# Kernel tuning notes

Hardware: AMD Instinct MI355X
Metric: run time of the kernel (lower is better)

Reference implementation:

```python
import jax, jax.numpy as jnp
import numpy as np

DIM = 768
NUM_HEADS = 12
HEAD_DIM = DIM // NUM_HEADS
H, W = 16, 64
HK, WK = 7, 11
N = H * W
B = 8
SCALE = HEAD_DIM ** -0.5


def build_local_mask():
    # Vectorized version of the original nested loop: for each token (h,w),
    # positions inside the hk x wk window are visible (0), others -inf.
    h_idx = np.repeat(np.arange(H), W)  # [N]
    w_idx = np.tile(np.arange(W), H)    # [N]
    hh = np.arange(H + HK - 1)
    ww = np.arange(W + WK - 1)
    in_h = (hh[None, :] >= h_idx[:, None]) & (hh[None, :] < h_idx[:, None] + HK)  # [N, H+hk-1]
    in_w = (ww[None, :] >= w_idx[:, None]) & (ww[None, :] < w_idx[:, None] + WK)  # [N, W+wk-1]
    visible = in_h[:, :, None] & in_w[:, None, :]  # [N, H+hk-1, W+wk-1]
    mask_big = np.where(visible, 0.0, 1.0).astype(np.float32)
    mask_crop = mask_big[:, HK // 2:H + HK // 2, WK // 2:W + WK // 2].reshape(N, N)
    mask = np.where(mask_crop < 1.0, mask_crop, np.float32(-np.inf))  # [N, N]
    return jnp.asarray(mask)[None, None]  # [1, 1, N, N]


def setup_inputs() -> dict:
    key = jax.random.key(0)
    k1, k2, k3 = jax.random.split(key, 3)
    x = jax.random.normal(k1, (B, N, DIM), dtype=jnp.float32)
    w_qkv = jax.random.normal(k2, (3 * DIM, DIM), dtype=jnp.float32) * 0.02  # torch Linear weight [out,in]
    w_proj = jax.random.normal(k3, (DIM, DIM), dtype=jnp.float32) * 0.02
    b_proj = jnp.zeros((DIM,), dtype=jnp.float32)
    mask = build_local_mask()
    return {"x": x, "w_qkv": w_qkv, "w_proj": w_proj, "b_proj": b_proj, "mask": mask}


def reference(x, w_qkv, w_proj, b_proj, mask):
    Bx, Nx, C = x.shape
    qkv = jnp.einsum('bnc,oc->bno', x, w_qkv)  # [B, N, 3*dim]
    qkv = qkv.reshape(Bx, Nx, 3, NUM_HEADS, HEAD_DIM).transpose(2, 0, 3, 1, 4)  # [3,B,h,N,d]
    q, k, v = qkv[0] * SCALE, qkv[1], qkv[2]
    attn = jnp.einsum('bhnd,bhmd->bhnm', q, k) + mask  # [B,h,N,N] with local -inf mask
    attn = jax.nn.softmax(attn, axis=-1)
    out = jnp.einsum('bhnm,bhmd->bhnd', attn, v)  # [B,h,N,d]
    out = out.transpose(0, 2, 1, 3).reshape(Bx, Nx, C)
    out = jnp.einsum('bnc,oc->bno', out, w_proj) + b_proj
    return out
```

## Files before the change

kernel.cpp:

```cpp
#include <hip/hip_runtime.h>
#include <hip/hip_bf16.h>
#include <stdint.h>

typedef __bf16 bf16;
typedef __bf16 bf16x8 __attribute__((ext_vector_type(8)));
typedef __bf16 bf16x4 __attribute__((ext_vector_type(4)));
typedef float f32x4 __attribute__((ext_vector_type(4)));

#define KDIM 768
#define NHEAD 12
#define HDIM 64
#define NTOK 1024
#define BATCH 8

#define SWZ(row, b) ((b) ^ (((row) & 7) << 4))

__device__ __forceinline__ void gl_lds16(const bf16* g, bf16* l) {
    __builtin_amdgcn_global_load_lds((const __attribute__((address_space(1))) void*)g,
                                     (__attribute__((address_space(3))) void*)l, 16, 0, 0);
}

#define G_MFMA(a, b, c) __builtin_amdgcn_mfma_f32_16x16x32_bf16(a, b, c, 0, 0, 0)
#define VMW(N) asm volatile("s_waitcnt vmcnt(" #N ")" ::: "memory")

__global__ void k_cvt_all(const float* __restrict__ x, const float* __restrict__ wq,
                          const float* __restrict__ wp, bf16* __restrict__ xb,
                          bf16* __restrict__ wqb, bf16* __restrict__ wpb) {
    int b = blockIdx.x;
    const float* src;
    bf16* dst;
    int base;
    if (b < 6144)       { src = x;  dst = xb;  base = b; }
    else if (b < 7872)  { src = wq; dst = wqb; base = b - 6144; }
    else                { src = wp; dst = wpb; base = b - 7872; }
    int i = (base * 256 + threadIdx.x) * 4;
    float4 v = *(const float4*)(src + i);
    bf16x4 o;
    o[0] = (bf16)v.x; o[1] = (bf16)v.y; o[2] = (bf16)v.z; o[3] = (bf16)v.w;
    *(bf16x4*)(dst + i) = o;
}


#define TILE64(S, kt) do {                                                      \
    const char* A8 = (const char*)sA[S];                                        \
    const char* B8 = (const char*)sB[S];                                        \
    bf16x8 af[4], bfr[6];                                                       \
    _Pragma("unroll")                                                           \
    for (int m = 0; m < 4; ++m)                                                 \
        af[m] = *(const bf16x8*)(A8 + (wr * 64 + m * 16 + lr) * 128 + k0off);   \
    _Pragma("unroll")                                                           \
    for (int n = 0; n < 6; ++n)                                                 \
        bfr[n] = *(const bf16x8*)(B8 + (wc * 96 + n * 16 + lr) * 128 + k0off);  \
    if ((kt) < 11) {                                                            \
        const bf16* p_ = Ast + (size_t)((kt) + 1) * 64;                         \
        gl_lds16(p_,                      &sA[(S) ^ 1][t * 8]);                 \
        gl_lds16(p_ + (size_t)32 * KDIM,  &sA[(S) ^ 1][t * 8 + 2048]);          \
        gl_lds16(p_ + (size_t)64 * KDIM,  &sA[(S) ^ 1][t * 8 + 4096]);          \
        gl_lds16(p_ + (size_t)96 * KDIM,  &sA[(S) ^ 1][t * 8 + 6144]);          \
    }                                                                           \
    __builtin_amdgcn_s_setprio(1);                                              \
    _Pragma("unroll")                                                           \
    for (int m = 0; m < 4; ++m)                                                 \
        _Pragma("unroll")                                                       \
        for (int n = 0; n < 6; ++n)                                             \
            acc[m][n] = G_MFMA(af[m], bfr[n], acc[m][n]);                       \
    __builtin_amdgcn_s_setprio(0);                                              \
    _Pragma("unroll")                                                           \
    for (int m = 0; m < 4; ++m)                                                 \
        af[m] = *(const bf16x8*)(A8 + (wr * 64 + m * 16 + lr) * 128 + k1off);   \
    _Pragma("unroll")                                                           \
    for (int n = 0; n < 6; ++n)                                                 \
        bfr[n] = *(const bf16x8*)(B8 + (wc * 96 + n * 16 + lr) * 128 + k1off);  \
    if ((kt) < 11) {                                                            \
        const bf16* p_ = Wst + (size_t)((kt) + 1) * 64;                         \
        gl_lds16(p_,                       &sB[(S) ^ 1][t * 8]);                \
        gl_lds16(p_ + (size_t)32 * KDIM,   &sB[(S) ^ 1][t * 8 + 2048]);         \
        gl_lds16(p_ + (size_t)64 * KDIM,   &sB[(S) ^ 1][t * 8 + 4096]);         \
        gl_lds16(p_ + (size_t)96 * KDIM,   &sB[(S) ^ 1][t * 8 + 6144]);         \
        gl_lds16(p_ + (size_t)128 * KDIM,  &sB[(S) ^ 1][t * 8 + 8192]);         \
        gl_lds16(p_ + (size_t)160 * KDIM,  &sB[(S) ^ 1][t * 8 + 10240]);        \
    }                                                                           \
    __builtin_amdgcn_s_setprio(1);                                              \
    _Pragma("unroll")                                                           \
    for (int m = 0; m < 4; ++m)                                                 \
        _Pragma("unroll")                                                       \
        for (int n = 0; n < 6; ++n)                                             \
            acc[m][n] = G_MFMA(af[m], bfr[n], acc[m][n]);                       \
    __builtin_amdgcn_s_setprio(0);                                              \
    VMW(0);                                                                     \
    __builtin_amdgcn_s_barrier();                                               \
} while (0)

#define GEMM64_PRE(A_PTR, W_PTR)                                                \
    const int t = threadIdx.x;                                                  \
    const int lane = t & 63;                                                    \
    const int wv = t >> 6;                                                      \
    const int wr = wv >> 1, wc = wv & 1;                                        \
    const int lr = lane & 15, lg = lane >> 4;                                   \
    const int xorb = (lr & 7) << 4;                                             \
    const int k0off = (lg << 4) ^ xorb;                                         \
    const int k1off = (64 + (lg << 4)) ^ xorb;                                  \
    const int spos = ((t & 7) ^ ((t >> 3) & 7)) * 8;                            \
    const int bm = blockIdx.x, bn = blockIdx.y;                                 \
    const bf16* Ast = (A_PTR) + (size_t)(bm * 128 + (t >> 3)) * KDIM + spos;    \
    const bf16* Wst = (W_PTR) + (size_t)(bn * 192 + (t >> 3)) * KDIM + spos;    \
    f32x4 acc[4][6] = {};                                                       \
    gl_lds16(Ast,                      &sA[0][t * 8]);                          \
    gl_lds16(Ast + (size_t)32 * KDIM,  &sA[0][t * 8 + 2048]);                   \
    gl_lds16(Ast + (size_t)64 * KDIM,  &sA[0][t * 8 + 4096]);                   \
    gl_lds16(Ast + (size_t)96 * KDIM,  &sA[0][t * 8 + 6144]);                   \
    gl_lds16(Wst,                       &sB[0][t * 8]);                         \
    gl_lds16(Wst + (size_t)32 * KDIM,   &sB[0][t * 8 + 2048]);                  \
    gl_lds16(Wst + (size_t)64 * KDIM,   &sB[0][t * 8 + 4096]);                  \
    gl_lds16(Wst + (size_t)96 * KDIM,   &sB[0][t * 8 + 6144]);                  \
    gl_lds16(Wst + (size_t)128 * KDIM,  &sB[0][t * 8 + 8192]);                  \
    gl_lds16(Wst + (size_t)160 * KDIM,  &sB[0][t * 8 + 10240]);                 \
    VMW(0);                                                                     \
    __builtin_amdgcn_s_barrier();                                               \
    _Pragma("unroll 1")                                                         \
    for (int g = 0; g < 6; ++g) {                                               \
        TILE64(0, g * 2);                                                       \
        TILE64(1, g * 2 + 1);                                                   \
    }

__global__ __launch_bounds__(256, 2) void k_gemm_qkv(
    const bf16* __restrict__ A, const bf16* __restrict__ W,
    bf16* __restrict__ qb, bf16* __restrict__ kb, bf16* __restrict__ vb)
{
    __shared__ __attribute__((aligned(16))) bf16 sA[2][8192];
    __shared__ __attribute__((aligned(16))) bf16 sB[2][12288];
    GEMM64_PRE(A, W);

    const float QSC = 0.18033688011112042f;
#pragma unroll
    for (int n = 0; n < 6; ++n) {
        int o = bn * 192 + wc * 96 + n * 16 + lr;
        int s = o / 768;
        int rem = o - s * 768;
        int head = rem >> 6;
        int d = o & 63;
        bf16* dst = (s == 0) ? qb : ((s == 1) ? kb : vb);
        float sc = (s == 0) ? QSC : 1.0f;
#pragma unroll
        for (int m = 0; m < 4; ++m) {
            int grow = bm * 128 + wr * 64 + m * 16 + lg * 4;
            int bidx = grow >> 10;
            int tok = grow & 1023;
            size_t base = (((size_t)bidx * NHEAD + head) * NTOK + tok) * HDIM + d;
#pragma unroll
            for (int r = 0; r < 4; ++r)
                dst[base + (size_t)r * HDIM] = (bf16)(acc[m][n][r] * sc);
        }
    }
}

__global__ __launch_bounds__(256, 2) void k_gemm_proj(
    const bf16* __restrict__ A, const bf16* __restrict__ W,
    const float* __restrict__ bias, float* __restrict__ out)
{
    __shared__ __attribute__((aligned(16))) bf16 sA[2][8192];
    __shared__ __attribute__((aligned(16))) bf16 sB[2][12288];
    GEMM64_PRE(A, W);

#pragma unroll
    for (int n = 0; n < 6; ++n) {
        int col = bn * 192 + wc * 96 + n * 16 + lr;
        float bv = bias[col];
#pragma unroll
        for (int m = 0; m < 4; ++m) {
            int grow = bm * 128 + wr * 64 + m * 16 + lg * 4;
#pragma unroll
            for (int r = 0; r < 4; ++r)
                out[(size_t)(grow + r) * KDIM + col] = acc[m][n][r] + bv;
        }
    }
}

__global__ __launch_bounds__(256) void k_attn(
    const bf16* __restrict__ qbuf, const bf16* __restrict__ kbuf,
    const bf16* __restrict__ vbuf, bf16* __restrict__ ob)
{
    const int x = blockIdx.x;
    const int sub = x >> 3;
    const int bh = (x & 7) * 12 + (sub >> 4);
    const int qblk = sub & 15;
    const int head = bh % NHEAD, bidx = bh / NHEAD;
    const bf16* Q  = qbuf + (size_t)bh * NTOK * HDIM;
    const bf16* Kp = kbuf + (size_t)bh * NTOK * HDIM;
    const bf16* Vp = vbuf + (size_t)bh * NTOK * HDIM;

    const int t = threadIdx.x, lane = t & 63, wv = t >> 6;
    const int lr = lane & 15, lg = lane >> 4, lkb = lg * 8;

    __shared__ bf16 Ks[2][64 * 64];
    __shared__ bf16 vT[2][64 * 64];
    __shared__ bf16 pls[4][16 * 64];

    {
        bf16x8 z = {};
        *(bf16x8*)&pls[wv][lane * 16] = z;
        *(bf16x8*)&pls[wv][lane * 16 + 8] = z;
    }

    bf16x8 qf[2];
#pragma unroll
    for (int ks = 0; ks < 2; ++ks)
        qf[ks] = *(const bf16x8*)(Q + (size_t)(qblk * 64 + wv * 16 + lr) * HDIM + ks * 32 + lkb);

    f32x4 acc[4] = {};
    float lrow[4] = {0.f, 0.f, 0.f, 0.f};

    const int kh0 = (qblk - 3 < 0) ? 0 : qblk - 3;
    const int kh1 = (qblk + 3 > 15) ? 15 : qblk + 3;

    const int sj = t >> 2;
    const int sd = (t & 3) * 16;

    const bf16* ks0 = Kp + (size_t)(kh0 * 64 + sj) * HDIM + sd;
    const bf16* vs0 = Vp + (size_t)(kh0 * 64 + sj) * HDIM + sd;
    bf16x8 gk0 = *(const bf16x8*)ks0, gk1 = *(const bf16x8*)(ks0 + 8);
    bf16x8 gv0 = *(const bf16x8*)vs0, gv1 = *(const bf16x8*)(vs0 + 8);

    char* pb8 = (char*)pls[wv];
    const int wq0 = wv * 16 + lg * 4;
    int cur = 0;

    for (int kh = kh0; kh <= kh1; ++kh) {
        char* kb8 = (char*)Ks[cur];
        char* vb8 = (char*)vT[cur];
        {
            int kbo = sj * 128 + sd * 2;
            *(bf16x8*)(kb8 + SWZ(sj, kbo)) = gk0;
            *(bf16x8*)(kb8 + SWZ(sj, kbo + 16)) = gk1;
        }
#pragma unroll
        for (int ii = 0; ii < 8; ++ii) {
            int d = sd + ii;
            *(bf16*)(vb8 + SWZ(d, (d << 7) + (sj << 1))) = gv0[ii];
        }
#pragma unroll
        for (int ii = 0; ii < 8; ++ii) {
            int d = sd + 8 + ii;
            *(bf16*)(vb8 + SWZ(d, (d << 7) + (sj << 1))) = gv1[ii];
        }
        if (kh < kh1) {
            const bf16* kn = Kp + (size_t)((kh + 1) * 64 + sj) * HDIM + sd;
            const bf16* vn = Vp + (size_t)((kh + 1) * 64 + sj) * HDIM + sd;
            gk0 = *(const bf16x8*)kn; gk1 = *(const bf16x8*)(kn + 8);
            gv0 = *(const bf16x8*)vn; gv1 = *(const bf16x8*)(vn + 8);
        }
        asm volatile("s_waitcnt lgkmcnt(0)" ::: "memory");
        __builtin_amdgcn_s_barrier();

        float psum[4] = {0.f, 0.f, 0.f, 0.f};
#pragma unroll
        for (int jj = 0; jj < 3; ++jj) {
            int j = wv - 1 + jj;
            if (j >= 0 && j <= 3) {
                int key = j * 16 + lr;
                int kbase = key * 128;
                bf16x8 kf0 = *(const bf16x8*)(kb8 + SWZ(key, kbase + lg * 16));
                bf16x8 kf1 = *(const bf16x8*)(kb8 + SWZ(key, kbase + 64 + lg * 16));
                f32x4 sv = {};
                sv = G_MFMA(qf[0], kf0, sv);
                sv = G_MFMA(qf[1], kf1, sv);
#pragma unroll
                for (int r = 0; r < 4; ++r) {
                    int dw = wq0 + r - key;
                    float p = (dw >= -5 && dw <= 5) ? exp2f(sv[r]) : 0.0f;
                    psum[r] += p;
                    int row = lg * 4 + r;
                    *(bf16*)(pb8 + SWZ(row, row * 128 + key * 2)) = (bf16)p;
                }
            }
        }
#pragma unroll
        for (int r = 0; r < 4; ++r) lrow[r] += psum[r];

        bf16x8 pf0 = *(const bf16x8*)(pb8 + SWZ(lr, lr * 128 + lg * 16));
        bf16x8 pf1 = *(const bf16x8*)(pb8 + SWZ(lr, lr * 128 + 64 + lg * 16));
#pragma unroll
        for (int dt = 0; dt < 4; ++dt) {
            int vrow = dt * 16 + lr;
            bf16x8 vf0 = *(const bf16x8*)(vb8 + SWZ(vrow, vrow * 128 + lg * 16));
            bf16x8 vf1 = *(const bf16x8*)(vb8 + SWZ(vrow, vrow * 128 + 64 + lg * 16));
            acc[dt] = G_MFMA(pf0, vf0, acc[dt]);
            acc[dt] = G_MFMA(pf1, vf1, acc[dt]);
        }
        cur ^= 1;
    }

#pragma unroll
    for (int off = 1; off < 16; off <<= 1)
#pragma unroll
        for (int r = 0; r < 4; ++r) lrow[r] += __shfl_xor(lrow[r], off);

#pragma unroll
    for (int r = 0; r < 4; ++r) {
        float inv = 1.0f / lrow[r];
        int tok = qblk * 64 + wv * 16 + lg * 4 + r;
        size_t rowbase = ((size_t)bidx * NTOK + tok) * KDIM + head * HDIM;
#pragma unroll
        for (int dt = 0; dt < 4; ++dt)
            ob[rowbase + dt * 16 + lr] = (bf16)(acc[dt][r] * inv);
    }
}

extern "C" void kernel_launch(void* const* d_in, const int* in_sizes, int n_in,
                              void* d_out, int out_size, void* d_ws, size_t ws_size,
                              hipStream_t stream) {
    const float* x      = (const float*)d_in[0];
    const float* w_qkv  = (const float*)d_in[1];
    const float* w_proj = (const float*)d_in[2];
    const float* b_proj = (const float*)d_in[3];
    float* out = (float*)d_out;

    char* ws = (char*)d_ws;
    bf16* xb  = (bf16*)(ws);
    bf16* wqb = (bf16*)(ws + 12582912);
    bf16* wpb = (bf16*)(ws + 16121856);
    bf16* qb  = (bf16*)(ws + 17301504);
    bf16* kb  = (bf16*)(ws + 29884416);
    bf16* vb  = (bf16*)(ws + 42467328);
    bf16* aob = (bf16*)(ws + 55050240);

    hipLaunchKernelGGL(k_cvt_all, dim3(8448), dim3(256), 0, stream, x, w_qkv, w_proj, xb, wqb, wpb);
    hipLaunchKernelGGL(k_gemm_qkv, dim3(64, 12), dim3(256), 0, stream, xb, wqb, qb, kb, vb);
    hipLaunchKernelGGL(k_attn,     dim3(1536), dim3(256), 0, stream, qb, kb, vb, aob);
    hipLaunchKernelGGL(k_gemm_proj, dim3(64, 4), dim3(256), 0, stream, aob, wpb, b_proj, out);
}
```

Before: 91.20 us.

## Process two query blocks per attention workgroup to share K/V tile loads

The attention kernel now uses 512-thread workgroups covering two adjacent 64-row query blocks, with eight waves split into two groups of four. Each K/V key block is loaded and transposed into LDS once and consumed by both query groups. This halves the grid and cuts redundant global K/V loads and LDS staging per query block. In exchange, the loop spans one extra key block, during which half the waves sit idle at the barrier. Occupancy may also change with the larger workgroup and LDS footprint.

```diff
diff --git a/kernel.cpp b/kernel.cpp
--- a/kernel.cpp
+++ b/kernel.cpp
@@ -176,25 +176,27 @@
     }
 }
 
-__global__ __launch_bounds__(256) void k_attn(
+__global__ __launch_bounds__(512) void k_attn(
     const bf16* __restrict__ qbuf, const bf16* __restrict__ kbuf,
     const bf16* __restrict__ vbuf, bf16* __restrict__ ob)
 {
     const int x = blockIdx.x;
     const int sub = x >> 3;
-    const int bh = (x & 7) * 12 + (sub >> 4);
-    const int qblk = sub & 15;
+    const int bh = (x & 7) * 12 + (sub >> 3);
+    const int qp = sub & 7;
     const int head = bh % NHEAD, bidx = bh / NHEAD;
     const bf16* Q  = qbuf + (size_t)bh * NTOK * HDIM;
     const bf16* Kp = kbuf + (size_t)bh * NTOK * HDIM;
     const bf16* Vp = vbuf + (size_t)bh * NTOK * HDIM;
 
     const int t = threadIdx.x, lane = t & 63, wv = t >> 6;
+    const int p4 = wv & 3;
+    const int myq = qp * 2 + (wv >> 2);
     const int lr = lane & 15, lg = lane >> 4, lkb = lg * 8;
 
-    __shared__ bf16 Ks[2][64 * 64];
-    __shared__ bf16 vT[2][64 * 64];
-    __shared__ bf16 pls[4][16 * 64];
+    __shared__ bf16 Ks[2][4096];
+    __shared__ bf16 vT[2][4096];
+    __shared__ bf16 pls[8][1024];
 
     {
         bf16x8 z = {};
@@ -205,87 +207,77 @@
     bf16x8 qf[2];
 #pragma unroll
     for (int ks = 0; ks < 2; ++ks)
-        qf[ks] = *(const bf16x8*)(Q + (size_t)(qblk * 64 + wv * 16 + lr) * HDIM + ks * 32 + lkb);
+        qf[ks] = *(const bf16x8*)(Q + (size_t)(myq * 64 + p4 * 16 + lr) * HDIM + ks * 32 + lkb);
 
     f32x4 acc[4] = {};
     float lrow[4] = {0.f, 0.f, 0.f, 0.f};
 
-    const int kh0 = (qblk - 3 < 0) ? 0 : qblk - 3;
-    const int kh1 = (qblk + 3 > 15) ? 15 : qblk + 3;
-
-    const int sj = t >> 2;
-    const int sd = (t & 3) * 16;
-
-    const bf16* ks0 = Kp + (size_t)(kh0 * 64 + sj) * HDIM + sd;
-    const bf16* vs0 = Vp + (size_t)(kh0 * 64 + sj) * HDIM + sd;
-    bf16x8 gk0 = *(const bf16x8*)ks0, gk1 = *(const bf16x8*)(ks0 + 8);
-    bf16x8 gv0 = *(const bf16x8*)vs0, gv1 = *(const bf16x8*)(vs0 + 8);
+    const int lo = (qp * 2 - 3 < 0) ? 0 : qp * 2 - 3;
+    const int hi = (qp * 2 + 4 > 15) ? 15 : qp * 2 + 4;
+
+    const int srow = t >> 3;
+    const int sch  = t & 7;
+
+    bf16x8 gk = *(const bf16x8*)(Kp + (size_t)(lo * 64 + srow) * HDIM + sch * 8);
+    bf16x8 gv = *(const bf16x8*)(Vp + (size_t)(lo * 64 + srow) * HDIM + sch * 8);
 
     char* pb8 = (char*)pls[wv];
-    const int wq0 = wv * 16 + lg * 4;
+    const int wq0 = p4 * 16 + lg * 4;
     int cur = 0;
 
-    for (int kh = kh0; kh <= kh1; ++kh) {
+#pragma unroll 1
+    for (int kh = lo; kh <= hi; ++kh) {
         char* kb8 = (char*)Ks[cur];
         char* vb8 = (char*)vT[cur];
-        {
-            int kbo = sj * 128 + sd * 2;
-            *(bf16x8*)(kb8 + SWZ(sj, kbo)) = gk0;
-            *(bf16x8*)(kb8 + SWZ(sj, kbo + 16)) = gk1;
-        }
-#pragma unroll
-        for (int ii = 0; ii < 8; ++ii) {
-            int d = sd + ii;
-            *(bf16*)(vb8 + SWZ(d, (d << 7) + (sj << 1))) = gv0[ii];
-        }
-#pragma unroll
-        for (int ii = 0; ii < 8; ++ii) {
-            int d = sd + 8 + ii;
-            *(bf16*)(vb8 + SWZ(d, (d << 7) + (sj << 1))) = gv1[ii];
-        }
-        if (kh < kh1) {
-            const bf16* kn = Kp + (size_t)((kh + 1) * 64 + sj) * HDIM + sd;
-            const bf16* vn = Vp + (size_t)((kh + 1) * 64 + sj) * HDIM + sd;
-            gk0 = *(const bf16x8*)kn; gk1 = *(const bf16x8*)(kn + 8);
-            gv0 = *(const bf16x8*)vn; gv1 = *(const bf16x8*)(vn + 8);
+        *(bf16x8*)(kb8 + SWZ(srow, srow * 128 + sch * 16)) = gk;
+#pragma unroll
+        for (int e = 0; e < 8; ++e) {
+            int d = sch * 8 + e;
+            *(bf16*)(vb8 + SWZ(d, (d << 7) + (srow << 1))) = gv[e];
+        }
+        if (kh < hi) {
+            gk = *(const bf16x8*)(Kp + (size_t)((kh + 1) * 64 + srow) * HDIM + sch * 8);
+            gv = *(const bf16x8*)(Vp + (size_t)((kh + 1) * 64 + srow) * HDIM + sch * 8);
         }
         asm volatile("s_waitcnt lgkmcnt(0)" ::: "memory");
         __builtin_amdgcn_s_barrier();
 
-        float psum[4] = {0.f, 0.f, 0.f, 0.f};
-#pragma unroll
-        for (int jj = 0; jj < 3; ++jj) {
-            int j = wv - 1 + jj;
-            if (j >= 0 && j <= 3) {
-                int key = j * 16 + lr;
-                int kbase = key * 128;
-                bf16x8 kf0 = *(const bf16x8*)(kb8 + SWZ(key, kbase + lg * 16));
-                bf16x8 kf1 = *(const bf16x8*)(kb8 + SWZ(key, kbase + 64 + lg * 16));
-                f32x4 sv = {};
-                sv = G_MFMA(qf[0], kf0, sv);
-                sv = G_MFMA(qf[1], kf1, sv);
-#pragma unroll
-                for (int r = 0; r < 4; ++r) {
-                    int dw = wq0 + r - key;
-                    float p = (dw >= -5 && dw <= 5) ? exp2f(sv[r]) : 0.0f;
-                    psum[r] += p;
-                    int row = lg * 4 + r;
-                    *(bf16*)(pb8 + SWZ(row, row * 128 + key * 2)) = (bf16)p;
+        if (kh >= myq - 3 && kh <= myq + 3) {
+            float psum[4] = {0.f, 0.f, 0.f, 0.f};
+#pragma unroll
+            for (int jj = 0; jj < 3; ++jj) {
+                int j = p4 - 1 + jj;
+                if (j >= 0 && j <= 3) {
+                    int key = j * 16 + lr;
+                    int kbase = key * 128;
+                    bf16x8 kf0 = *(const bf16x8*)(kb8 + SWZ(key, kbase + lg * 16));
+                    bf16x8 kf1 = *(const bf16x8*)(kb8 + SWZ(key, kbase + 64 + lg * 16));
+                    f32x4 sv = {};
+                    sv = G_MFMA(qf[0], kf0, sv);
+                    sv = G_MFMA(qf[1], kf1, sv);
+#pragma unroll
+                    for (int r = 0; r < 4; ++r) {
+                        int dw = wq0 + r - key;
+                        float p = (dw >= -5 && dw <= 5) ? exp2f(sv[r]) : 0.0f;
+                        psum[r] += p;
+                        int row = lg * 4 + r;
+                        *(bf16*)(pb8 + SWZ(row, row * 128 + key * 2)) = (bf16)p;
+                    }
                 }
             }
-        }
-#pragma unroll
-        for (int r = 0; r < 4; ++r) lrow[r] += psum[r];
-
-        bf16x8 pf0 = *(const bf16x8*)(pb8 + SWZ(lr, lr * 128 + lg * 16));
-        bf16x8 pf1 = *(const bf16x8*)(pb8 + SWZ(lr, lr * 128 + 64 + lg * 16));
-#pragma unroll
-        for (int dt = 0; dt < 4; ++dt) {
-            int vrow = dt * 16 + lr;
-            bf16x8 vf0 = *(const bf16x8*)(vb8 + SWZ(vrow, vrow * 128 + lg * 16));
-            bf16x8 vf1 = *(const bf16x8*)(vb8 + SWZ(vrow, vrow * 128 + 64 + lg * 16));
-            acc[dt] = G_MFMA(pf0, vf0, acc[dt]);
-            acc[dt] = G_MFMA(pf1, vf1, acc[dt]);
+#pragma unroll
+            for (int r = 0; r < 4; ++r) lrow[r] += psum[r];
+
+            bf16x8 pf0 = *(const bf16x8*)(pb8 + SWZ(lr, lr * 128 + lg * 16));
+            bf16x8 pf1 = *(const bf16x8*)(pb8 + SWZ(lr, lr * 128 + 64 + lg * 16));
+#pragma unroll
+            for (int dt = 0; dt < 4; ++dt) {
+                int vrow = dt * 16 + lr;
+                bf16x8 vf0 = *(const bf16x8*)(vb8 + SWZ(vrow, vrow * 128 + lg * 16));
+                bf16x8 vf1 = *(const bf16x8*)(vb8 + SWZ(vrow, vrow * 128 + 64 + lg * 16));
+                acc[dt] = G_MFMA(pf0, vf0, acc[dt]);
+                acc[dt] = G_MFMA(pf1, vf1, acc[dt]);
+            }
         }
         cur ^= 1;
     }
@@ -298,7 +290,7 @@
 #pragma unroll
     for (int r = 0; r < 4; ++r) {
         float inv = 1.0f / lrow[r];
-        int tok = qblk * 64 + wv * 16 + lg * 4 + r;
+        int tok = myq * 64 + p4 * 16 + lg * 4 + r;
         size_t rowbase = ((size_t)bidx * NTOK + tok) * KDIM + head * HDIM;
 #pragma unroll
         for (int dt = 0; dt < 4; ++dt)
@@ -326,6 +318,6 @@
 
     hipLaunchKernelGGL(k_cvt_all, dim3(8448), dim3(256), 0, stream, x, w_qkv, w_proj, xb, wqb, wpb);
     hipLaunchKernelGGL(k_gemm_qkv, dim3(64, 12), dim3(256), 0, stream, xb, wqb, qb, kb, vb);
-    hipLaunchKernelGGL(k_attn,     dim3(1536), dim3(256), 0, stream, qb, kb, vb, aob);
+    hipLaunchKernelGGL(k_attn,     dim3(768), dim3(512), 0, stream, qb, kb, vb, aob);
     hipLaunchKernelGGL(k_gemm_proj, dim3(64, 4), dim3(256), 0, stream, aob, wpb, b_proj, out);
 }
```

Measured after the change: 94.91 us. 4.1% more time.
